# Kernel tuning notes

Hardware: AMD Instinct MI355X
Metric: run time of the kernel (lower is better)

The kernel has to match this reference:

```python
import jax, jax.numpy as jnp
from jax import lax
import numpy as np


def setup_inputs() -> dict:
    key = jax.random.key(0)
    ks = iter(jax.random.split(key, 48))

    def w(shape):
        fan = shape[0] if len(shape) == 2 else int(np.prod(shape[1:]))
        return jax.random.normal(next(ks), shape, jnp.float32) / np.sqrt(fan)

    def b(n):
        return jax.random.normal(next(ks), (n,), jnp.float32) * 0.01

    T = 16
    return dict(
        search=jax.random.normal(next(ks), (3, 383, 287), jnp.float32),
        exemplars=jax.random.normal(next(ks), (T, 3, 383, 287), jnp.float32),
        # AlexNet features (random-weight stand-in for pretrained)
        aw1=w((64, 3, 11, 11)), ab1=b(64),
        aw2=w((192, 64, 5, 5)), ab2=b(192),
        aw3=w((384, 192, 3, 3)), ab3=b(384),
        aw4=w((256, 384, 3, 3)), ab4=b(256),
        aw5=w((256, 256, 3, 3)), ab5=b(256),
        # conv_deconv: Conv1d(256,256,3,p=1) -> MaxPool1d(88) -> ConvTranspose1d(256,256,88)
        wcd=w((256, 256, 3)), bcd=b(256),
        wt=w((256, 256, 88)), bt=b(256),
        # st_gcn: GCN(256, 512, 256)
        ws1=w((256, 512)), bs1=b(512),
        ws2=w((512, 256)), bs2=b(256),
        # g, h: 1x1 Conv1d(256,256) == linear maps
        wg=w((256, 256)), bg=b(256),
        wh=w((256, 256)), bh=b(256),
        # ct_gcn: GCN(256, 384, 256)
        wc1=w((256, 384)), bc1=b(384),
        wc2=w((384, 256)), bc2=b(256),
    )


def _gct_forward(search, exemplars, aw1, ab1, aw2, ab2, aw3, ab3, aw4, ab4,
                 aw5, ab5, wcd, bcd, wt, bt, ws1, bs1, ws2, bs2,
                 wg, bg, wh, bh, wc1, bc1, wc2, bc2):
    f32 = jnp.float32

    def conv2d(x, w, bias, s, p):
        y = lax.conv_general_dilated(x, w, (s, s), [(p, p), (p, p)],
                                     dimension_numbers=('NCHW', 'OIHW', 'NCHW'))
        return y + bias[None, :, None, None]

    def maxpool(x):  # k=3, s=2, VALID (AlexNet pools)
        return lax.reduce_window(x, -jnp.inf, lax.max, (1, 1, 3, 3), (1, 1, 2, 2), 'VALID')

    def features(x):
        x = maxpool(jax.nn.relu(conv2d(x, aw1, ab1, 4, 2)))
        x = maxpool(jax.nn.relu(conv2d(x, aw2, ab2, 1, 2)))
        x = jax.nn.relu(conv2d(x, aw3, ab3, 1, 1))
        x = jax.nn.relu(conv2d(x, aw4, ab4, 1, 1))
        x = maxpool(jax.nn.relu(conv2d(x, aw5, ab5, 1, 1)))
        return x

    lrelu = lambda v: jax.nn.leaky_relu(v, 0.01)

    X = features(search[None])          # [1,256,11,8]
    Z = features(exemplars)             # [T,256,11,8]
    T = Z.shape[0]
    D = X.shape[1]                      # 256
    M = X.shape[2] * X.shape[3]         # 88
    Xf = X.reshape(D, M)                # [256,88]
    Zf = Z.reshape(T, D, M)             # [T,256,88]

    # conv_deconv branch: conv1d(k=3,p=1) -> global maxpool -> conv_transpose(k=M)
    xc = lax.conv_general_dilated(Xf[None], wcd, (1,), [(1, 1)],
                                  dimension_numbers=('NCH', 'OIH', 'NCH'))[0] + bcd[:, None]
    v = jnp.max(xc, axis=1)                              # [256]
    X_hat = jnp.einsum('i,iok->ok', v, wt) + bt[:, None]  # [256,88]

    # spatiotemporal graph: A[i+T*j, i+T*k]=1 for j!=k; self-loops for t!=0
    TM = T * M
    n = jnp.arange(TM)
    same_t = (n[:, None] % T) == (n[None, :] % T)
    diff_s = (n[:, None] // T) != (n[None, :] // T)
    A1 = (same_t & diff_s).astype(f32) + jnp.diag((n % T != 0).astype(f32))

    # st GCN over TM nodes (node n = t + T*m -> spatial-major flatten)
    nodes = Zf.transpose(2, 0, 1).reshape(TM, D)          # [TM,256]
    h1 = lrelu(A1 @ (nodes @ ws1) + bs1)                  # [TM,512]
    h2 = lrelu(A1 @ (h1 @ ws2) + bs2)                     # [TM,256]
    V1 = jnp.max(h2.reshape(M, T, D), axis=1).T           # temporal max-pool -> [256,88]

    # dynamic cross-track graph: pairwise g/h affinities + row softmax (fused)
    Vx = V1 + X_hat                                       # [256,88]
    G = wg @ Vx + bg[:, None]                             # [256,88]
    Hh = wh @ Vx + bh[:, None]                            # [256,88]
    A2 = jax.nn.softmax(Hh.T @ G, axis=1)                 # [88,88], A2[j,i]=g(i).h(j)

    # ct GCN
    xv = V1.T                                             # [88,256]
    c1 = lrelu(A2 @ (xv @ wc1) + bc1)                     # [88,384]
    V2 = lrelu(A2 @ (c1 @ wc2) + bc2).T                   # [256,88]

    # F.conv2d(X[1,256,11,8], V2[1,256,11,8]) -> full-overlap correlation = scalar
    R = jnp.sum(Xf * V2).reshape(1, 1, 1, 1)
    return R


def reference(search, exemplars, aw1, ab1, aw2, ab2, aw3, ab3, aw4, ab4,
              aw5, ab5, wcd, bcd, wt, bt, ws1, bs1, ws2, bs2,
              wg, bg, wh, bh, wc1, bc1, wc2, bc2):
    return _gct_forward(search, exemplars, aw1, ab1, aw2, ab2, aw3, ab3, aw4, ab4,
                        aw5, ab5, wcd, bcd, wt, bt, ws1, bs1, ws2, bs2,
                        wg, bg, wh, bh, wc1, bc1, wc2, bc2)
```

## Files before the change

kernel.cpp:

```cpp
#include <hip/hip_runtime.h>
#include <hip/hip_bf16.h>
#include <math.h>

#define BATCH 17
#define T_EX 16
#define H0 383
#define W0 287
#define C1 64
#define H1 95
#define W1 71
#define H1P 47
#define W1P 35
#define C2 192
#define H2P 23
#define W2P 17
#define C3 384
#define C45 256
#define H5P 11
#define W5P 8
#define DD 256
#define MM 88
#define TM 1408

#define HP1 389
#define WP1 292

typedef unsigned short ushort_t;
typedef __attribute__((ext_vector_type(8))) short short8;
typedef __attribute__((ext_vector_type(4))) float f32x4;

__device__ __forceinline__ float lrelu(float v) { return v > 0.f ? v : 0.01f * v; }

__device__ __forceinline__ ushort_t f2bf(float f) {
    unsigned int u = __float_as_uint(f);
    unsigned int r = (u + 0x7fffu + ((u >> 16) & 1u)) >> 16;
    return (ushort_t)r;
}
__device__ __forceinline__ float b2f(ushort_t b) {
    return __uint_as_float(((unsigned int)b) << 16);
}
__device__ __forceinline__ short8 ld16(const ushort_t* p) { return *(const short8*)p; }
__device__ __forceinline__ short8 ld2x8(const ushort_t* p) {
    union { uint2 u[2]; short8 s; } uu;
    uu.u[0] = *(const uint2*)p;
    uu.u[1] = *(const uint2*)(p + 4);
    return uu.s;
}
__device__ __forceinline__ void async_cp16(ushort_t* l, const ushort_t* g) {
    __builtin_amdgcn_global_load_lds(
        (const __attribute__((address_space(1))) void*)g,
        (__attribute__((address_space(3))) void*)l, 16, 0, 0);
}

__device__ __forceinline__ void wprep_dev(const float* __restrict__ w,
                                          ushort_t* __restrict__ out,
                                          int KH, int KWl, int KWr, int CINl, int CINr,
                                          int NKS, int OCr, int idx) {
    int c = idx & 255;
    int rest = idx >> 8;
    int ks = rest % NKS;
    int ocb = rest / NKS;
    int k8 = c >> 6, m = c & 63;
    int oc = ocb * 64 + m;
    int KWC = KWl * CINl;
    ushort_t* o = out + (size_t)idx * 8;
#pragma unroll
    for (int j = 0; j < 8; ++j) {
        int kg = ks * 32 + k8 * 8 + j;
        int ky = kg / KWC; int rem = kg - ky * KWC;
        int kx = rem / CINl; int ic = rem - kx * CINl;
        float v = 0.f;
        if (oc < OCr && ky < KH && kx < KWr && ic < CINr)
            v = w[(((size_t)oc * CINr + ic) * KH + ky) * KWr + kx];
        o[j] = f2bf(v);
    }
}

__global__ void prep1_wp1_k(const float* __restrict__ search, const float* __restrict__ exemp,
                            ushort_t* __restrict__ out, const float* __restrict__ w1,
                            ushort_t* __restrict__ WT) {
    const int pb = (BATCH * HP1 * WP1 + 255) / 256;
    if ((int)blockIdx.x >= pb) {
        int idx = (blockIdx.x - pb) * 256 + threadIdx.x;
        if (idx < 4608) wprep_dev(w1, WT, 11, 12, 11, 4, 3, 18, 64, idx);
        return;
    }
    int idx = blockIdx.x * 256 + threadIdx.x;
    if (idx >= BATCH * HP1 * WP1) return;
    int x = idx % WP1; int t = idx / WP1;
    int y = t % HP1; int b = t / HP1;
    ushort4 o = {0, 0, 0, 0};
    int ix = x - 2, iy = y - 2;
    if (ix >= 0 && ix < W0 && iy >= 0 && iy < H0) {
        const float* src = (b == 0) ? search : exemp + (size_t)(b - 1) * 3 * H0 * W0;
        const int hw = H0 * W0;
        o.x = f2bf(src[iy * W0 + ix]);
        o.y = f2bf(src[hw + iy * W0 + ix]);
        o.z = f2bf(src[2 * hw + iy * W0 + ix]);
    }
    *(ushort4*)&out[(size_t)idx * 4] = o;
}

__global__ void wprep_k(const float* __restrict__ w, ushort_t* __restrict__ out,
                        int KH, int KWl, int KWr, int CINl, int CINr,
                        int NKS, int nch, int OCr,
                        float4* __restrict__ zp, int zn4) {
    const int wb = (nch + 255) >> 8;
    if ((int)blockIdx.x >= wb) {
        int z = (blockIdx.x - wb) * 256 + threadIdx.x;
        if (z < zn4) zp[z] = (float4){0.f, 0.f, 0.f, 0.f};
        return;
    }
    int idx = blockIdx.x * 256 + threadIdx.x;
    if (idx >= nch) return;
    wprep_dev(w, out, KH, KWl, KWr, CINl, CINr, NKS, OCr, idx);
}

__global__ void pool_wp_k(const ushort_t* __restrict__ in, ushort_t* __restrict__ out,
                          int C, int Hin, int Win, int Hout, int Wout,
                          int OHp, int OWp, int OPAD,
                          float4* __restrict__ zp, int zn4,
                          const float* __restrict__ w, ushort_t* __restrict__ WT,
                          int KH, int KWl, int KWr, int CINl, int CINr,
                          int NKS, int nch, int OCr) {
    const int total = BATCH * C * OHp * OWp;
    const int pb = (total + 255) >> 8;
    const int zb = (zn4 + 255) >> 8;
    int bx = blockIdx.x;
    if (bx >= pb + zb) {
        int idx = (bx - pb - zb) * 256 + threadIdx.x;
        if (idx < nch) wprep_dev(w, WT, KH, KWl, KWr, CINl, CINr, NKS, OCr, idx);
        return;
    }
    if (bx >= pb) {
        int z = (bx - pb) * 256 + threadIdx.x;
        if (z < zn4) zp[z] = (float4){0.f, 0.f, 0.f, 0.f};
        return;
    }
    int idx = bx * 256 + threadIdx.x;
    if (idx >= total) return;
    int c = idx % C; int r = idx / C;
    int x = r % OWp; r /= OWp;
    int y = r % OHp; int b = r / OHp;
    int iy = y - OPAD, ix = x - OPAD;
    ushort_t v = 0;
    if (iy >= 0 && iy < Hout && ix >= 0 && ix < Wout) {
        const int rs = Win * C;
        const ushort_t* p = in + (((size_t)b * Hin + 2 * iy) * Win + 2 * ix) * C + c;
        float m = b2f(p[0]);
        m = fmaxf(m, b2f(p[C])); m = fmaxf(m, b2f(p[2 * C]));
        m = fmaxf(m, b2f(p[rs])); m = fmaxf(m, b2f(p[rs + C])); m = fmaxf(m, b2f(p[rs + 2 * C]));
        m = fmaxf(m, b2f(p[2 * rs])); m = fmaxf(m, b2f(p[2 * rs + C])); m = fmaxf(m, b2f(p[2 * rs + 2 * C]));
        v = f2bf(m);
    }
    out[idx] = v;
}

template <int STRIDE, bool A16>
__global__ __launch_bounds__(256) void conv_mfma14(
    const ushort_t* __restrict__ inp, const ushort_t* __restrict__ wt,
    const float* __restrict__ bias, ushort_t* __restrict__ out,
    int Hp, int Wp, int C, int Wout, int HW, int Ntot, int NKS2, int KWl,
    int OHp, int OWp, int OPAD, int COUT) {
    const int tid = threadIdx.x;
    const int wv = tid >> 6, lane = tid & 63;
    const int quad = lane >> 4, l16 = lane & 15;
    const int wr = wv >> 1, wc = wv & 1;
    const int n_blk = blockIdx.x * 64;
    const int ocb = blockIdx.y;

    __shared__ ushort_t As[2][4096];
    __shared__ ushort_t Bs[2][4096];
    __shared__ int offs[432];

    const int KWC = KWl * C;
    for (int g = tid; g < NKS2 * 8; g += 256) {
        int kg = g * 8;
        int ky = kg / KWC; int rem = kg - ky * KWC;
        int kx = rem / C; int c8 = rem - kx * C;
        offs[g] = (ky * Wp + kx) * C + c8;
    }

    const size_t HWC = (size_t)Hp * Wp * C;
    const int g8 = lane & 7, po = lane >> 3;
    const ushort_t* bsrc0 = nullptr; const ushort_t* bsrc1 = nullptr;
    const ushort_t* lsrc = nullptr;
    int ws0 = 0, ws1 = 0;
    if constexpr (A16) {
        int np0 = n_blk + wv * 16 + po;      if (np0 >= Ntot) np0 = Ntot - 1;
        int np1 = n_blk + wv * 16 + 8 + po;  if (np1 >= Ntot) np1 = Ntot - 1;
        int b0 = np0 / HW, p0 = np0 - b0 * HW;
        int b1 = np1 / HW, p1 = np1 - b1 * HW;
        int oy0 = p0 / Wout, ox0 = p0 - oy0 * Wout;
        int oy1 = p1 / Wout, ox1 = p1 - oy1 * Wout;
        bsrc0 = inp + (size_t)b0 * HWC + (size_t)(oy0 * STRIDE * Wp + ox0 * STRIDE) * C;
        bsrc1 = inp + (size_t)b1 * HWC + (size_t)(oy1 * STRIDE * Wp + ox1 * STRIDE) * C;
        ws0 = g8 * 512 + (((wv * 16 + po) ^ g8) * 8);
        ws1 = g8 * 512 + (((wv * 16 + 8 + po) ^ g8) * 8);
    } else {
        int n0 = n_blk + lane; if (n0 >= Ntot) n0 = Ntot - 1;
        int b0 = n0 / HW, p0 = n0 - b0 * HW;
        int oy = p0 / Wout, ox = p0 - oy * Wout;
        lsrc = inp + (size_t)b0 * HWC + (size_t)(oy * STRIDE * Wp + ox * STRIDE) * C;
    }

    f32x4 acc[2][2];
#pragma unroll
    for (int am = 0; am < 2; ++am)
#pragma unroll
        for (int bn = 0; bn < 2; ++bn) acc[am][bn] = (f32x4){0.f, 0.f, 0.f, 0.f};

    const ushort_t* wblk = wt + (size_t)ocb * (size_t)NKS2 * 4096;

    __syncthreads();

    {
        const ushort_t* aS = wblk + tid * 8;
        async_cp16(&As[0][tid * 8], aS);
        async_cp16(&As[0][2048 + tid * 8], aS + 2048);
        if constexpr (A16) {
            *(short8*)&Bs[0][ws0] = ld16(bsrc0 + offs[g8]);
            *(short8*)&Bs[0][ws1] = ld16(bsrc1 + offs[g8]);
        } else {
            const int o0 = offs[wv], o1 = offs[4 + wv];
            *(short8*)&Bs[0][tid * 8] = ld2x8(lsrc + o0);
            *(short8*)&Bs[0][2048 + tid * 8] = ld2x8(lsrc + o1);
        }
    }
    __syncthreads();

    for (int ks2 = 0; ks2 < NKS2; ++ks2) {
        const int cur = ks2 & 1, nxt = cur ^ 1;
        const bool more = (ks2 + 1 < NKS2);
        short8 rb0, rb1;
        if (more) {
            const ushort_t* aS = wblk + (size_t)(ks2 + 1) * 4096 + tid * 8;
            async_cp16(&As[nxt][tid * 8], aS);
            async_cp16(&As[nxt][2048 + tid * 8], aS + 2048);
            if constexpr (A16) {
                rb0 = ld16(bsrc0 + offs[(ks2 + 1) * 8 + g8]);
                rb1 = ld16(bsrc1 + offs[(ks2 + 1) * 8 + g8]);
            } else {
                const int o0 = offs[(ks2 + 1) * 8 + wv], o1 = offs[(ks2 + 1) * 8 + 4 + wv];
                *(short8*)&Bs[nxt][tid * 8] = ld2x8(lsrc + o0);
                *(short8*)&Bs[nxt][2048 + tid * 8] = ld2x8(lsrc + o1);
            }
        }
#pragma unroll
        for (int h = 0; h < 2; ++h) {
            const short8 a0 = *(const short8*)&As[cur][h * 2048 + (quad * 64 + wr * 32 + l16) * 8];
            const short8 a1 = *(const short8*)&As[cur][h * 2048 + (quad * 64 + wr * 32 + 16 + l16) * 8];
            short8 b0, b1;
            if constexpr (A16) {
                b0 = *(const short8*)&Bs[cur][h * 2048 + quad * 512 + (((wc * 32 + l16) ^ (h * 4 + quad)) * 8)];
                b1 = *(const short8*)&Bs[cur][h * 2048 + quad * 512 + (((wc * 32 + 16 + l16) ^ (h * 4 + quad)) * 8)];
            } else {
                b0 = *(const short8*)&Bs[cur][h * 2048 + (quad * 64 + wc * 32 + l16) * 8];
                b1 = *(const short8*)&Bs[cur][h * 2048 + (quad * 64 + wc * 32 + 16 + l16) * 8];
            }
            acc[0][0] = __builtin_amdgcn_mfma_f32_16x16x32_bf16(a0, b0, acc[0][0], 0, 0, 0);
            acc[0][1] = __builtin_amdgcn_mfma_f32_16x16x32_bf16(a0, b1, acc[0][1], 0, 0, 0);
            acc[1][0] = __builtin_amdgcn_mfma_f32_16x16x32_bf16(a1, b0, acc[1][0], 0, 0, 0);
            acc[1][1] = __builtin_amdgcn_mfma_f32_16x16x32_bf16(a1, b1, acc[1][1], 0, 0, 0);
        }
        if constexpr (A16) {
            if (more) {
                *(short8*)&Bs[nxt][ws0] = rb0;
                *(short8*)&Bs[nxt][ws1] = rb1;
            }
        }
        __syncthreads();
    }

    const int oc0 = ocb * 64 + wr * 32 + quad * 4;
#pragma unroll
    for (int bn = 0; bn < 2; ++bn) {
        int n = n_blk + wc * 32 + bn * 16 + l16;
        if (n < Ntot) {
            int bb = n / HW; int pix = n - bb * HW;
            int y = pix / Wout, x = pix - y * Wout;
            size_t base = (((size_t)bb * OHp + y + OPAD) * OWp + x + OPAD) * COUT;
#pragma unroll
            for (int am = 0; am < 2; ++am) {
                const int oc = oc0 + am * 16;
                ushort4 o;
                o.x = f2bf(fmaxf(acc[am][bn][0] + bias[oc], 0.f));
                o.y = f2bf(fmaxf(acc[am][bn][1] + bias[oc + 1], 0.f));
                o.z = f2bf(fmaxf(acc[am][bn][2] + bias[oc + 2], 0.f));
                o.w = f2bf(fmaxf(acc[am][bn][3] + bias[oc + 3], 0.f));
                *(ushort4*)&out[base + oc] = o;
            }
        }
    }
}

template <int MODE, bool HASBIAS, bool SC1>
__device__ __forceinline__ void gemm_dev(
    ushort_t (*Bs)[2048],
    const ushort_t* __restrict__ Bsrc, const ushort_t* __restrict__ wt,
    const float* __restrict__ bias, float* __restrict__ out,
    int RS, int N, int NKS, int sn, int sc, int bx, int by) {
    const int tid = threadIdx.x;
    const int wv = tid >> 6, lane = tid & 63;
    const int quad = lane >> 4, l16 = lane & 15;
    const int n_blk = bx * 64;
    const int ocb = by;

    int n_g = n_blk + lane;
    int n_gc = n_g < N ? n_g : N - 1;
    int row = (MODE == 1) ? (1 + (n_gc & 15)) * MM + (n_gc >> 4) : n_gc;
    const size_t base0 = (size_t)row * RS;

    f32x4 acc[4];
#pragma unroll
    for (int cn = 0; cn < 4; ++cn) acc[cn] = (f32x4){0.f, 0.f, 0.f, 0.f};

    const ushort_t* wblk = wt + (size_t)ocb * NKS * 2048;
    const int afrag = (quad * 64 + wv * 16 + l16) * 8;

    short8 a0 = ld16(wblk + afrag);
    *(short8*)&Bs[0][tid * 8] = ld16(Bsrc + base0 + wv * 8);
    __syncthreads();

    for (int ks = 0; ks < NKS; ++ks) {
        const int cur = ks & 1, nxt = cur ^ 1;
        short8 a1, bn;
        const bool more = (ks + 1 < NKS);
        if (more) {
            a1 = ld16(wblk + (ks + 1) * 2048 + afrag);
            bn = ld16(Bsrc + base0 + (ks + 1) * 32 + wv * 8);
        }
#pragma unroll
        for (int cn = 0; cn < 4; ++cn) {
            const short8 bfr = *(const short8*)&Bs[cur][(quad * 64 + cn * 16 + l16) * 8];
            acc[cn] = __builtin_amdgcn_mfma_f32_16x16x32_bf16(a0, bfr, acc[cn], 0, 0, 0);
        }
        if (more) *(short8*)&Bs[nxt][tid * 8] = bn;
        a0 = a1;
        __syncthreads();
    }

    const int oc0 = ocb * 64 + wv * 16 + quad * 4;
    float bb[4] = {0.f, 0.f, 0.f, 0.f};
    if (HASBIAS) { bb[0] = bias[oc0]; bb[1] = bias[oc0+1]; bb[2] = bias[oc0+2]; bb[3] = bias[oc0+3]; }
#pragma unroll
    for (int cn = 0; cn < 4; ++cn) {
        int n = n_blk + cn * 16 + l16;
        if (n < N) {
            if (SC1) {
                float4 o;
                o.x = acc[cn][0] + bb[0]; o.y = acc[cn][1] + bb[1];
                o.z = acc[cn][2] + bb[2]; o.w = acc[cn][3] + bb[3];
                *(float4*)&out[(size_t)n * sn + oc0] = o;
            } else {
#pragma unroll
                for (int reg = 0; reg < 4; ++reg)
                    out[(size_t)n * sn + (size_t)(oc0 + reg) * sc] = acc[cn][reg] + bb[reg];
            }
        }
    }
}

template <int MODE, bool HASBIAS, bool SC1>
__global__ __launch_bounds__(256) void gemm_mfma3_k(
    const ushort_t* __restrict__ Bsrc, const ushort_t* __restrict__ wt,
    const float* __restrict__ bias, float* __restrict__ out,
    int RS, int N, int NKS, int sn, int sc) {
    __shared__ ushort_t Bs[2][2048];
    gemm_dev<MODE, HASBIAS, SC1>(Bs, Bsrc, wt, bias, out, RS, N, NKS, sn, sc,
                                 blockIdx.x, blockIdx.y);
}

__global__ __launch_bounds__(256) void gemm_pair_k(
    const ushort_t* __restrict__ XfPad, const ushort_t* __restrict__ WCDT,
    const float* __restrict__ bcd, float* __restrict__ xc,
    const ushort_t* __restrict__ PB, const ushort_t* __restrict__ WS1T,
    float* __restrict__ Y1) {
    __shared__ ushort_t Bs[2][2048];
    if (blockIdx.x < 2) {
        if (blockIdx.y < 4)
            gemm_dev<0, true, false>(Bs, XfPad, WCDT, bcd, xc, 256, MM, 24, 1, MM,
                                     blockIdx.x, blockIdx.y);
    } else {
        gemm_dev<1, false, true>(Bs, PB, WS1T, nullptr, Y1, 256, TM, 8, 512, 1,
                                 blockIdx.x - 2, blockIdx.y);
    }
}

__global__ void wg_pool5_k(const float* __restrict__ ws1, const float* __restrict__ ws2,
                           const float* __restrict__ wcd, ushort_t* __restrict__ WS1T,
                           ushort_t* __restrict__ WS2T, ushort_t* __restrict__ WCDT,
                           const ushort_t* __restrict__ in, float* __restrict__ P,
                           ushort_t* __restrict__ PB, ushort_t* __restrict__ XfPad) {
    if (blockIdx.x < 224) {
        int idx = blockIdx.x * 256 + threadIdx.x;
        const float* src; ushort_t* dst; int NKS, mode = 0, sa = 1, sk = 0, base;
        if (idx < 16384)       { src = ws1; dst = WS1T; NKS = 8;  sk = 512; base = idx; }
        else if (idx < 32768)  { src = ws2; dst = WS2T; NKS = 16; sk = 256; base = idx - 16384; }
        else                   { src = wcd; dst = WCDT; NKS = 24; mode = 1; base = idx - 32768; }
        int c = base & 255;
        int rest = base >> 8;
        int ks = rest % NKS;
        int ocb = rest / NKS;
        int k8 = c >> 6, m = c & 63;
        int oc = ocb * 64 + m;
        ushort_t* o = dst + (size_t)base * 8;
#pragma unroll
        for (int j = 0; j < 8; ++j) {
            int kg = ks * 32 + k8 * 8 + j;
            float v;
            if (mode == 0) v = src[(size_t)oc * sa + (size_t)kg * sk];
            else           v = src[(size_t)oc * 768 + (kg & 255) * 3 + (kg >> 8)];
            o[j] = f2bf(v);
        }
    } else {
        int idx = (blockIdx.x - 224) * 256 + threadIdx.x;
        if (idx >= BATCH * 256 * MM) return;
        int c = idx % 256; int r = idx / 256;
        int x = r % W5P; r /= W5P;
        int y = r % H5P; int b = r / H5P;
        const int rs = W2P * 256;
        const ushort_t* p = in + (((size_t)b * H2P + 2 * y) * W2P + 2 * x) * 256 + c;
        float m = b2f(p[0]);
        m = fmaxf(m, b2f(p[256])); m = fmaxf(m, b2f(p[512]));
        m = fmaxf(m, b2f(p[rs])); m = fmaxf(m, b2f(p[rs + 256])); m = fmaxf(m, b2f(p[rs + 512]));
        m = fmaxf(m, b2f(p[2 * rs])); m = fmaxf(m, b2f(p[2 * rs + 256])); m = fmaxf(m, b2f(p[2 * rs + 512]));
        int mm = y * W5P + x;
        size_t o = ((size_t)b * MM + mm) * 256 + c;
        P[o] = m;
        ushort_t mb = f2bf(m);
        PB[o] = mb;
        if (b == 0) XfPad[(size_t)(mm + 1) * 256 + c] = mb;
    }
}

__global__ __launch_bounds__(1024) void xhat_sh1_k(
    const float* __restrict__ xc, const float* __restrict__ wt,
    const float* __restrict__ bt, float* __restrict__ xhat,
    const float* __restrict__ Y1, const float* __restrict__ bs1,
    ushort_t* __restrict__ h1b) {
    int tid = threadIdx.x;
    if (blockIdx.x < 22) {
        __shared__ float lv[256];
        if (tid < 256) {
            const float* xr = xc + (size_t)tid * MM;
            float mx = xr[0];
            for (int k = 1; k < MM; ++k) mx = fmaxf(mx, xr[k]);
            lv[tid] = mx;
        }
        __syncthreads();
        int idx = blockIdx.x * 1024 + tid;
        if (idx >= DD * MM) return;
        int k = idx % MM, o = idx / MM;
        float acc = bt[o];
        for (int i = 0; i < 256; ++i) acc = fmaf(lv[i], wt[(i * 256 + o) * MM + k], acc);
        xhat[idx] = acc;
    } else {
        int idx = (blockIdx.x - 22) * 1024 + tid;
        if (idx >= T_EX * 512) return;
        int c = idx & 511, t = idx >> 9;
        float s = 0.f;
        for (int m = 0; m < MM; ++m) s += Y1[(size_t)(m * T_EX + t) * 512 + c];
        float base = s + bs1[c];
        if (t == 0) {
            for (int m = 0; m < MM; ++m) {
                float val = base - Y1[(size_t)(m * T_EX) * 512 + c];
                h1b[(size_t)(m * T_EX) * 512 + c] = f2bf(lrelu(val));
            }
        } else {
            ushort_t v = f2bf(lrelu(base));
            for (int m = 0; m < MM; ++m)
                h1b[(size_t)(m * T_EX + t) * 512 + c] = v;
        }
    }
}

__global__ void sh2_k(const float* __restrict__ Y2, const float* __restrict__ bs2,
                      float* __restrict__ h2) {
    int idx = blockIdx.x * 256 + threadIdx.x;
    if (idx >= T_EX * 256) return;
    int c = idx & 255, t = idx >> 8;
    float s = 0.f;
    for (int m = 0; m < MM; ++m) s += Y2[(size_t)(m * T_EX + t) * 256 + c];
    float base = s + bs2[c];
    if (t == 0) {
        for (int m = 0; m < MM; ++m)
            h2[(size_t)(m * T_EX) * 256 + c] = lrelu(base - Y2[(size_t)(m * T_EX) * 256 + c]);
    } else {
        float v = lrelu(base);
        for (int m = 0; m < MM; ++m) h2[(size_t)(m * T_EX + t) * 256 + c] = v;
    }
}

__global__ __launch_bounds__(1024) void v1vx_k(
    const float* __restrict__ h2, const float* __restrict__ xhat,
    float* __restrict__ V1, float* __restrict__ Vx) {
    int idx = blockIdx.x * 1024 + threadIdx.x;
    if (idx >= DD * MM) return;
    int m = idx % MM, d = idx / MM;
    float mx = -INFINITY;
    for (int t = 0; t < T_EX; ++t) mx = fmaxf(mx, h2[(m * T_EX + t) * 256 + d]);
    V1[idx] = mx;
    Vx[idx] = mx + xhat[idx];
}

__global__ __launch_bounds__(1024) void lin_t1_k(
    const float* __restrict__ Wgm, const float* __restrict__ bg,
    const float* __restrict__ Whm, const float* __restrict__ bh,
    const float* __restrict__ Vx, float* __restrict__ G,
    float* __restrict__ Hh,
    const float* __restrict__ V1, const float* __restrict__ wc1,
    float* __restrict__ t1) {
    int bx = blockIdx.x;
    int tid = threadIdx.x;
    if (bx < 44) {
        int sel = bx >= 22;
        int idx = (bx - (sel ? 22 : 0)) * 1024 + tid;
        if (idx >= DD * MM) return;
        const float* W = sel ? Whm : Wgm;
        const float* bias = sel ? bh : bg;
        float* out = sel ? Hh : G;
        int m = idx % MM, o = idx / MM;
        const float* wr = W + o * 256;
        float acc = bias[o];
        for (int i = 0; i < 256; ++i) acc = fmaf(wr[i], Vx[i * MM + m], acc);
        out[idx] = acc;
    } else {
        int idx = (bx - 44) * 1024 + tid;
        if (idx >= MM * 384) return;
        int c = idx % 384, m = idx / 384;
        float acc = 0.f;
        for (int d = 0; d < 256; ++d) acc = fmaf(V1[d * MM + m], wc1[d * 384 + c], acc);
        t1[idx] = acc;
    }
}

__global__ void smsm_k(const float* __restrict__ Hh, const float* __restrict__ G,
                       float* __restrict__ A2) {
    int j = blockIdx.x;
    int tid = threadIdx.x;
    __shared__ float row[96];
    __shared__ float red[128];
    for (int i = tid; i < MM; i += 128) {
        float acc = 0.f;
        for (int c = 0; c < 256; ++c) acc = fmaf(Hh[c * MM + j], G[c * MM + i], acc);
        row[i] = acc;
    }
    __syncthreads();
    float val = (tid < MM) ? row[tid] : -INFINITY;
    red[tid] = val; __syncthreads();
    for (int s = 64; s > 0; s >>= 1) {
        if (tid < s) red[tid] = fmaxf(red[tid], red[tid + s]);
        __syncthreads();
    }
    float mx = red[0]; __syncthreads();
    float e = (tid < MM) ? expf(val - mx) : 0.f;
    red[tid] = e; __syncthreads();
    for (int s = 64; s > 0; s >>= 1) {
        if (tid < s) red[tid] += red[tid + s];
        __syncthreads();
    }
    float inv = 1.f / red[0];
    if (tid < MM) A2[j * MM + tid] = e * inv;
}

__global__ __launch_bounds__(1024) void c1_k(
    const float* __restrict__ A2, const float* __restrict__ t1,
    const float* __restrict__ bc1, float* __restrict__ c1) {
    int idx = blockIdx.x * 1024 + threadIdx.x;
    if (idx >= MM * 384) return;
    int c = idx % 384, j = idx / 384;
    float acc = bc1[c];
    for (int i = 0; i < MM; ++i) acc = fmaf(A2[j * MM + i], t1[i * 384 + c], acc);
    c1[idx] = lrelu(acc);
}

__global__ __launch_bounds__(1024) void t2_k(
    const float* __restrict__ c1, const float* __restrict__ wc2,
    float* __restrict__ t2) {
    int idx = blockIdx.x * 1024 + threadIdx.x;
    if (idx >= MM * 256) return;
    int c = idx % 256, m = idx / 256;
    const float* cr = c1 + m * 384;
    float acc = 0.f;
    for (int d = 0; d < 384; ++d) acc = fmaf(cr[d], wc2[d * 256 + c], acc);
    t2[idx] = acc;
}

__global__ __launch_bounds__(1024) void v2_k(
    const float* __restrict__ A2, const float* __restrict__ t2,
    const float* __restrict__ bc2, float* __restrict__ V2m) {
    int idx = blockIdx.x * 1024 + threadIdx.x;
    if (idx >= MM * 256) return;
    int c = idx % 256, j = idx / 256;
    float acc = bc2[c];
    for (int i = 0; i < MM; ++i) acc = fmaf(A2[j * MM + i], t2[i * 256 + c], acc);
    V2m[idx] = lrelu(acc);
}

__global__ void final_k(const float* __restrict__ Xf2, const float* __restrict__ V2m,
                        float* __restrict__ out) {
    __shared__ float red[256];
    float acc = 0.f;
    for (int idx = threadIdx.x; idx < DD * MM; idx += 256)
        acc = fmaf(Xf2[idx], V2m[idx], acc);
    red[threadIdx.x] = acc; __syncthreads();
    for (int s = 128; s > 0; s >>= 1) {
        if (threadIdx.x < s) red[threadIdx.x] += red[threadIdx.x + s];
        __syncthreads();
    }
    if (threadIdx.x == 0) out[0] = red[0];
}

extern "C" void kernel_launch(void* const* d_in, const int* in_sizes, int n_in,
                              void* d_out, int out_size, void* d_ws, size_t ws_size,
                              hipStream_t stream) {
    const float* search = (const float*)d_in[0];
    const float* exemp  = (const float*)d_in[1];
    const float* aw1 = (const float*)d_in[2];  const float* ab1 = (const float*)d_in[3];
    const float* aw2 = (const float*)d_in[4];  const float* ab2 = (const float*)d_in[5];
    const float* aw3 = (const float*)d_in[6];  const float* ab3 = (const float*)d_in[7];
    const float* aw4 = (const float*)d_in[8];  const float* ab4 = (const float*)d_in[9];
    const float* aw5 = (const float*)d_in[10]; const float* ab5 = (const float*)d_in[11];
    const float* wcd = (const float*)d_in[12]; const float* bcd = (const float*)d_in[13];
    const float* wt  = (const float*)d_in[14]; const float* bt  = (const float*)d_in[15];
    const float* ws1 = (const float*)d_in[16]; const float* bs1 = (const float*)d_in[17];
    const float* ws2 = (const float*)d_in[18]; const float* bs2 = (const float*)d_in[19];
    const float* wg  = (const float*)d_in[20]; const float* bg  = (const float*)d_in[21];
    const float* wh  = (const float*)d_in[22]; const float* bh  = (const float*)d_in[23];
    const float* wc1 = (const float*)d_in[24]; const float* bc1 = (const float*)d_in[25];
    const float* wc2 = (const float*)d_in[26]; const float* bc2 = (const float*)d_in[27];

    float* ws = (float*)d_ws;
    float* R1 = ws;
    float* R2 = ws + 3870720;
    float* R3 = ws + 7544832;
    float* Wg = ws + 8628864;

    ushort_t* in1p  = (ushort_t*)R1;
    ushort_t* c1out = (ushort_t*)R2;
    ushort_t* p1out = (ushort_t*)R3;
    ushort_t* c2out = (ushort_t*)R1;
    ushort_t* p2out = (ushort_t*)R2;
    ushort_t* c3out = (ushort_t*)(R2 + 775200);
    ushort_t* c4out = (ushort_t*)R1;
    ushort_t* c5out = (ushort_t*)R3;
    ushort_t* WT    = (ushort_t*)Wg;

    prep1_wp1_k<<<7543 + 18, 256, 0, stream>>>(search, exemp, in1p, aw1, WT);
    conv_mfma14<4, false><<<dim3(1792, 1), 256, 0, stream>>>(
        in1p, WT, ab1, c1out, HP1, WP1, 4, W1, H1 * W1, BATCH * H1 * W1, 9, 12, H1, W1, 0, 64);
    pool_wp_k<<<8454 + 150, 256, 0, stream>>>(
        c1out, p1out, 64, H1, W1, H1P, W1P, 51, 39, 2, nullptr, 0,
        aw2, WT, 5, 5, 5, 64, 64, 50, 38400, 192);
    conv_mfma14<1, true><<<dim3(437, 3), 256, 0, stream>>>(
        p1out, WT, ab2, c2out, 51, 39, 64, W1P, H1P * W1P, BATCH * H1P * W1P, 25, 5, H1P, W1P, 0, 192);
    pool_wp_k<<<6057 + 1515 + 324, 256, 0, stream>>>(
        c2out, p2out, 192, H1P, W1P, H2P, W2P, 25, 19, 1,
        (float4*)(R2 + 775200), 387600,
        aw3, WT, 3, 3, 3, 192, 192, 54, 82944, 384);
    conv_mfma14<1, true><<<dim3(104, 6), 256, 0, stream>>>(
        p2out, WT, ab3, c3out, 25, 19, 192, W2P, H2P * W2P, BATCH * H2P * W2P, 27, 3, 25, 19, 1, 384);
    wprep_k<<<432 + 1010, 256, 0, stream>>>(aw4, WT, 3, 3, 3, 384, 384, 108, 110592, 256,
                                            (float4*)R1, 258400);
    conv_mfma14<1, true><<<dim3(104, 4), 256, 0, stream>>>(
        c3out, WT, ab4, c4out, 25, 19, 384, W2P, H2P * W2P, BATCH * H2P * W2P, 54, 3, 25, 19, 1, 256);
    wprep_k<<<288, 256, 0, stream>>>(aw5, WT, 3, 3, 3, 256, 256, 72, 73728, 256, nullptr, 0);
    conv_mfma14<1, true><<<dim3(104, 4), 256, 0, stream>>>(
        c4out, WT, ab5, c5out, 25, 19, 256, W2P, H2P * W2P, BATCH * H2P * W2P, 36, 3, H2P, W2P, 0, 256);

    float*    P      = R1 + 2417664;
    ushort_t* PB     = (ushort_t*)(R1 + 2800640);
    ushort_t* XfPad  = (ushort_t*)(R1 + 2992128);
    float*    xc     = R1 + 3003648;

    ushort_t* WS1T = (ushort_t*)Wg;
    ushort_t* WS2T = (ushort_t*)(Wg + 65536);
    ushort_t* WCDT = (ushort_t*)(Wg + 131072);

    wg_pool5_k<<<224 + (BATCH * 256 * MM + 255) / 256, 256, 0, stream>>>(
        ws1, ws2, wcd, WS1T, WS2T, WCDT, c5out, P, PB, XfPad);
    float* Xf2 = P;

    float* xhat = R1 + 1024;
    float* Y1   = R1 + 23552;
    ushort_t* h1b = (ushort_t*)(R1 + 752640);
    float* Y2   = R1 + 1473536;
    float* h2   = R1 + 1838080;
    float* V1   = R1 + 2198528;
    float* Vx   = R1 + 2221056;
    float* G    = R1 + 2243584;
    float* Hh   = R1 + 2266112;
    float* A2   = R1 + 2296832;
    float* t1   = R1 + 2305024;
    float* c1   = R1 + 2338816;
    float* t2   = R1 + 2372608;
    float* V2m  = R1 + 2395136;

    gemm_pair_k<<<dim3(24, 8), 256, 0, stream>>>(XfPad, WCDT, bcd, xc, PB, WS1T, Y1);
    xhat_sh1_k<<<30, 1024, 0, stream>>>(xc, wt, bt, xhat, Y1, bs1, h1b);

    gemm_mfma3_k<0, false, true><<<dim3(22, 4), 256, 0, stream>>>(
        h1b, WS2T, nullptr, Y2, 512, TM, 16, 256, 1);
    sh2_k<<<16, 256, 0, stream>>>(Y2, bs2, h2);
    v1vx_k<<<22, 1024, 0, stream>>>(h2, xhat, V1, Vx);

    lin_t1_k<<<77, 1024, 0, stream>>>(wg, bg, wh, bh, Vx, G, Hh, V1, wc1, t1);
    smsm_k<<<MM, 128, 0, stream>>>(Hh, G, A2);

    c1_k<<<33, 1024, 0, stream>>>(A2, t1, bc1, c1);
    t2_k<<<22, 1024, 0, stream>>>(c1, wc2, t2);
    v2_k<<<22, 1024, 0, stream>>>(A2, t2, bc2, V2m);

    final_k<<<1, 256, 0, stream>>>(Xf2, V2m, (float*)d_out);
}
```

Measured before the change: 487.9 us.

## Fuse GCN tail kernels, shrink blocks to 256 threads, use last-block reduction

```diff
diff --git a/kernel.cpp b/kernel.cpp
--- a/kernel.cpp
+++ b/kernel.cpp
@@ -434,29 +434,28 @@
     }
 }
 
-__global__ __launch_bounds__(1024) void xhat_sh1_k(
-    const float* __restrict__ xc, const float* __restrict__ wt,
-    const float* __restrict__ bt, float* __restrict__ xhat,
-    const float* __restrict__ Y1, const float* __restrict__ bs1,
-    ushort_t* __restrict__ h1b) {
-    int tid = threadIdx.x;
-    if (blockIdx.x < 22) {
+__global__ void xhat_sh1_k(const float* __restrict__ xc, const float* __restrict__ wt,
+                           const float* __restrict__ bt, float* __restrict__ xhat,
+                           const float* __restrict__ Y1, const float* __restrict__ bs1,
+                           ushort_t* __restrict__ h1b) {
+    if (blockIdx.x < 88) {
         __shared__ float lv[256];
-        if (tid < 256) {
-            const float* xr = xc + (size_t)tid * MM;
+        {
+            int j = threadIdx.x;
+            const float* xr = xc + (size_t)j * MM;
             float mx = xr[0];
             for (int k = 1; k < MM; ++k) mx = fmaxf(mx, xr[k]);
-            lv[tid] = mx;
+            lv[j] = mx;
         }
         __syncthreads();
-        int idx = blockIdx.x * 1024 + tid;
+        int idx = blockIdx.x * 256 + threadIdx.x;
         if (idx >= DD * MM) return;
         int k = idx % MM, o = idx / MM;
         float acc = bt[o];
         for (int i = 0; i < 256; ++i) acc = fmaf(lv[i], wt[(i * 256 + o) * MM + k], acc);
         xhat[idx] = acc;
     } else {
-        int idx = (blockIdx.x - 22) * 1024 + tid;
+        int idx = (blockIdx.x - 88) * 256 + threadIdx.x;
         if (idx >= T_EX * 512) return;
         int c = idx & 511, t = idx >> 9;
         float s = 0.f;
@@ -475,47 +474,41 @@
     }
 }
 
-__global__ void sh2_k(const float* __restrict__ Y2, const float* __restrict__ bs2,
-                      float* __restrict__ h2) {
-    int idx = blockIdx.x * 256 + threadIdx.x;
-    if (idx >= T_EX * 256) return;
-    int c = idx & 255, t = idx >> 8;
-    float s = 0.f;
-    for (int m = 0; m < MM; ++m) s += Y2[(size_t)(m * T_EX + t) * 256 + c];
-    float base = s + bs2[c];
-    if (t == 0) {
-        for (int m = 0; m < MM; ++m)
-            h2[(size_t)(m * T_EX) * 256 + c] = lrelu(base - Y2[(size_t)(m * T_EX) * 256 + c]);
-    } else {
-        float v = lrelu(base);
-        for (int m = 0; m < MM; ++m) h2[(size_t)(m * T_EX + t) * 256 + c] = v;
-    }
-}
-
-__global__ __launch_bounds__(1024) void v1vx_k(
-    const float* __restrict__ h2, const float* __restrict__ xhat,
-    float* __restrict__ V1, float* __restrict__ Vx) {
-    int idx = blockIdx.x * 1024 + threadIdx.x;
-    if (idx >= DD * MM) return;
-    int m = idx % MM, d = idx / MM;
-    float mx = -INFINITY;
-    for (int t = 0; t < T_EX; ++t) mx = fmaxf(mx, h2[(m * T_EX + t) * 256 + d]);
-    V1[idx] = mx;
-    Vx[idx] = mx + xhat[idx];
-}
-
-__global__ __launch_bounds__(1024) void lin_t1_k(
-    const float* __restrict__ Wgm, const float* __restrict__ bg,
-    const float* __restrict__ Whm, const float* __restrict__ bh,
-    const float* __restrict__ Vx, float* __restrict__ G,
-    float* __restrict__ Hh,
-    const float* __restrict__ V1, const float* __restrict__ wc1,
-    float* __restrict__ t1) {
+__global__ void sh2v1_k(const float* __restrict__ Y2, const float* __restrict__ bs2,
+                        const float* __restrict__ xhat,
+                        float* __restrict__ V1, float* __restrict__ Vx) {
+    int d = blockIdx.x;
+    int tid = threadIdx.x;
+    __shared__ float S2s[16];
+    if (tid < 16) {
+        float s = 0.f;
+        for (int m = 0; m < MM; ++m) s += Y2[(size_t)(m * T_EX + tid) * 256 + d];
+        S2s[tid] = s + bs2[d];
+    }
+    __syncthreads();
+    for (int m = tid; m < MM; m += 128) {
+        float y0 = Y2[(size_t)(m * T_EX) * 256 + d];
+        float mx = -INFINITY;
+        for (int t = 0; t < T_EX; ++t) {
+            float val = (t == 0) ? lrelu(S2s[0] - y0) : lrelu(S2s[t]);
+            mx = fmaxf(mx, val);
+        }
+        int idx = d * MM + m;
+        V1[idx] = mx;
+        Vx[idx] = mx + xhat[idx];
+    }
+}
+
+__global__ void lin_t1_k(const float* __restrict__ Wgm, const float* __restrict__ bg,
+                         const float* __restrict__ Whm, const float* __restrict__ bh,
+                         const float* __restrict__ Vx, float* __restrict__ G,
+                         float* __restrict__ Hh,
+                         const float* __restrict__ V1, const float* __restrict__ wc1,
+                         float* __restrict__ t1) {
     int bx = blockIdx.x;
-    int tid = threadIdx.x;
-    if (bx < 44) {
-        int sel = bx >= 22;
-        int idx = (bx - (sel ? 22 : 0)) * 1024 + tid;
+    if (bx < 176) {
+        int sel = bx >= 88;
+        int idx = (bx - (sel ? 88 : 0)) * 256 + threadIdx.x;
         if (idx >= DD * MM) return;
         const float* W = sel ? Whm : Wgm;
         const float* bias = sel ? bh : bg;
@@ -526,7 +519,7 @@
         for (int i = 0; i < 256; ++i) acc = fmaf(wr[i], Vx[i * MM + m], acc);
         out[idx] = acc;
     } else {
-        int idx = (bx - 44) * 1024 + tid;
+        int idx = (bx - 176) * 256 + threadIdx.x;
         if (idx >= MM * 384) return;
         int c = idx % 384, m = idx / 384;
         float acc = 0.f;
@@ -564,10 +557,11 @@
     if (tid < MM) A2[j * MM + tid] = e * inv;
 }
 
-__global__ __launch_bounds__(1024) void c1_k(
-    const float* __restrict__ A2, const float* __restrict__ t1,
-    const float* __restrict__ bc1, float* __restrict__ c1) {
-    int idx = blockIdx.x * 1024 + threadIdx.x;
+__global__ void c1_k(const float* __restrict__ A2, const float* __restrict__ t1,
+                     const float* __restrict__ bc1, float* __restrict__ c1,
+                     unsigned* __restrict__ cnt) {
+    if (blockIdx.x == 0 && threadIdx.x == 0) *cnt = 0u;
+    int idx = blockIdx.x * 256 + threadIdx.x;
     if (idx >= MM * 384) return;
     int c = idx % 384, j = idx / 384;
     float acc = bc1[c];
@@ -575,10 +569,9 @@
     c1[idx] = lrelu(acc);
 }
 
-__global__ __launch_bounds__(1024) void t2_k(
-    const float* __restrict__ c1, const float* __restrict__ wc2,
-    float* __restrict__ t2) {
-    int idx = blockIdx.x * 1024 + threadIdx.x;
+__global__ void t2_k(const float* __restrict__ c1, const float* __restrict__ wc2,
+                     float* __restrict__ t2) {
+    int idx = blockIdx.x * 256 + threadIdx.x;
     if (idx >= MM * 256) return;
     int c = idx % 256, m = idx / 256;
     const float* cr = c1 + m * 384;
@@ -587,29 +580,42 @@
     t2[idx] = acc;
 }
 
-__global__ __launch_bounds__(1024) void v2_k(
-    const float* __restrict__ A2, const float* __restrict__ t2,
-    const float* __restrict__ bc2, float* __restrict__ V2m) {
-    int idx = blockIdx.x * 1024 + threadIdx.x;
-    if (idx >= MM * 256) return;
-    int c = idx % 256, j = idx / 256;
-    float acc = bc2[c];
-    for (int i = 0; i < MM; ++i) acc = fmaf(A2[j * MM + i], t2[i * 256 + c], acc);
-    V2m[idx] = lrelu(acc);
-}
-
-__global__ void final_k(const float* __restrict__ Xf2, const float* __restrict__ V2m,
-                        float* __restrict__ out) {
-    __shared__ float red[256];
-    float acc = 0.f;
-    for (int idx = threadIdx.x; idx < DD * MM; idx += 256)
-        acc = fmaf(Xf2[idx], V2m[idx], acc);
-    red[threadIdx.x] = acc; __syncthreads();
-    for (int s = 128; s > 0; s >>= 1) {
-        if (threadIdx.x < s) red[threadIdx.x] += red[threadIdx.x + s];
-        __syncthreads();
-    }
-    if (threadIdx.x == 0) out[0] = red[0];
+__global__ __launch_bounds__(256) void v2f_k(const float* __restrict__ A2,
+                                             const float* __restrict__ t2,
+                                             const float* __restrict__ bc2,
+                                             const float* __restrict__ Xf2,
+                                             float* __restrict__ V2m,
+                                             unsigned* __restrict__ cnt,
+                                             float* __restrict__ out) {
+    int j = blockIdx.x;
+    int tid = threadIdx.x;
+    __shared__ float a2row[88];
+    if (tid < 88) a2row[tid] = A2[j * MM + tid];
+    __syncthreads();
+    {
+        int c = tid;
+        float acc = bc2[c];
+        for (int i = 0; i < MM; ++i) acc = fmaf(a2row[i], t2[i * 256 + c], acc);
+        V2m[(size_t)j * 256 + c] = lrelu(acc);
+    }
+    __threadfence();
+    __syncthreads();
+    __shared__ bool last;
+    if (tid == 0) last = (atomicAdd(cnt, 1u) == 87u);
+    __syncthreads();
+    if (last) {
+        __threadfence();
+        __shared__ float red[256];
+        float acc = 0.f;
+        for (int idx = tid; idx < DD * MM; idx += 256)
+            acc = fmaf(Xf2[idx], V2m[idx], acc);
+        red[tid] = acc; __syncthreads();
+        for (int s = 128; s > 0; s >>= 1) {
+            if (tid < s) red[tid] += red[tid + s];
+            __syncthreads();
+        }
+        if (tid == 0) out[0] = red[0];
+    }
 }
 
 extern "C" void kernel_launch(void* const* d_in, const int* in_sizes, int n_in,
@@ -686,7 +692,6 @@
     float* Y1   = R1 + 23552;
     ushort_t* h1b = (ushort_t*)(R1 + 752640);
     float* Y2   = R1 + 1473536;
-    float* h2   = R1 + 1838080;
     float* V1   = R1 + 2198528;
     float* Vx   = R1 + 2221056;
     float* G    = R1 + 2243584;
@@ -696,21 +701,19 @@
     float* c1   = R1 + 2338816;
     float* t2   = R1 + 2372608;
     float* V2m  = R1 + 2395136;
+    unsigned* cnt = (unsigned*)(R1 + 512);
 
     gemm_pair_k<<<dim3(24, 8), 256, 0, stream>>>(XfPad, WCDT, bcd, xc, PB, WS1T, Y1);
-    xhat_sh1_k<<<30, 1024, 0, stream>>>(xc, wt, bt, xhat, Y1, bs1, h1b);
+    xhat_sh1_k<<<120, 256, 0, stream>>>(xc, wt, bt, xhat, Y1, bs1, h1b);
 
     gemm_mfma3_k<0, false, true><<<dim3(22, 4), 256, 0, stream>>>(
         h1b, WS2T, nullptr, Y2, 512, TM, 16, 256, 1);
-    sh2_k<<<16, 256, 0, stream>>>(Y2, bs2, h2);
-    v1vx_k<<<22, 1024, 0, stream>>>(h2, xhat, V1, Vx);
-
-    lin_t1_k<<<77, 1024, 0, stream>>>(wg, bg, wh, bh, Vx, G, Hh, V1, wc1, t1);
+    sh2v1_k<<<256, 128, 0, stream>>>(Y2, bs2, xhat, V1, Vx);
+
+    lin_t1_k<<<308, 256, 0, stream>>>(wg, bg, wh, bh, Vx, G, Hh, V1, wc1, t1);
     smsm_k<<<MM, 128, 0, stream>>>(Hh, G, A2);
 
-    c1_k<<<33, 1024, 0, stream>>>(A2, t1, bc1, c1);
-    t2_k<<<22, 1024, 0, stream>>>(c1, wc2, t2);
-    v2_k<<<22, 1024, 0, stream>>>(A2, t2, bc2, V2m);
-
-    final_k<<<1, 256, 0, stream>>>(Xf2, V2m, (float*)d_out);
-}
+    c1_k<<<132, 256, 0, stream>>>(A2, t1, bc1, c1, cnt);
+    t2_k<<<88, 256, 0, stream>>>(c1, wc2, t2);
+    v2f_k<<<MM, 256, 0, stream>>>(A2, t2, bc2, Xf2, V2m, cnt, (float*)d_out);
+}
```

Result: faster. 457.6 us (-6.2%).
